# Kernel tuning notes

Hardware: AMD Instinct MI355X
Metric: run time of the kernel (lower is better)

## Reference

```python
import jax, jax.numpy as jnp
import numpy as np

B, C, H, W = 2, 128, 32, 48
D_INNER = 2 * C          # expand=2
D_STATE = 16
DT_RANK = int(np.ceil(C / 16))
K = 4                    # four scan directions
EPS = 1e-5


def setup_inputs() -> dict:
    ks = jax.random.split(jax.random.key(0), 8)
    return {
        "rgb": jax.random.normal(ks[0], (B, C, H, W), jnp.float32),
        "t": jax.random.normal(ks[1], (B, C, H, W), jnp.float32),
        "in_proj_w": jax.random.normal(ks[2], (2 * D_INNER, C), jnp.float32) / np.float32(np.sqrt(C)),
        "conv_w": jax.random.normal(ks[3], (D_INNER, 1, 3, 3), jnp.float32) / 3.0,
        "conv_b": jnp.zeros((D_INNER,), jnp.float32),
        "x_proj_w": jax.random.normal(ks[4], (K, DT_RANK + 2 * D_STATE, D_INNER), jnp.float32) / np.float32(np.sqrt(D_INNER)),
        "dt_projs_w": jax.random.normal(ks[5], (K, D_INNER, DT_RANK), jnp.float32) * np.float32(DT_RANK ** -0.5),
        "dt_projs_b": jax.random.uniform(ks[6], (K, D_INNER), jnp.float32, minval=1e-4, maxval=0.1),
        "A_logs": jnp.log(jnp.tile(jnp.arange(1, D_STATE + 1, dtype=jnp.float32), (K * D_INNER, 1))),
        "Ds": jnp.ones((K * D_INNER,), jnp.float32),
        "out_norm_g": jnp.ones((D_INNER,), jnp.float32),
        "out_norm_b": jnp.zeros((D_INNER,), jnp.float32),
        "out_proj_w": jax.random.normal(ks[7], (C, D_INNER), jnp.float32) / np.float32(np.sqrt(D_INNER)),
    }


def _selective_scan(u, delta, A, Bmat, Cmat, Dvec):
    """u, delta: (B,K,D,L); A: (K,D,N); Bmat/Cmat: (B,K,N,L); Dvec: (K,D)."""
    uT = jnp.moveaxis(u, -1, 0)      # (L,B,K,D)
    dT = jnp.moveaxis(delta, -1, 0)  # (L,B,K,D)
    BT = jnp.moveaxis(Bmat, -1, 0)   # (L,B,K,N)
    CT = jnp.moveaxis(Cmat, -1, 0)   # (L,B,K,N)
    h0 = jnp.zeros(u.shape[:3] + (A.shape[-1],), u.dtype)  # (B,K,D,N)

    def step(h, xs):
        u_t, d_t, B_t, C_t = xs
        dA = jnp.exp(d_t[..., None] * A)                       # (B,K,D,N)
        h = dA * h + (d_t * u_t)[..., None] * B_t[:, :, None, :]
        y = jnp.einsum('bkdn,bkn->bkd', h, C_t)
        return h, y

    _, ys = jax.lax.scan(step, h0, (uT, dT, BT, CT))           # ys: (L,B,K,D)
    return jnp.moveaxis(ys, 0, -1) + Dvec[None, :, :, None] * u


def _ss2d(x, in_proj_w, conv_w, conv_b, x_proj_w, dt_projs_w, dt_projs_b,
          A_logs, Ds, out_norm_g, out_norm_b, out_proj_w):
    b, hs, ws, c = x.shape
    L = hs * ws
    xz = x @ in_proj_w.T                                       # (B,Hs,Ws,2*Din)
    xx, z = jnp.split(xz, 2, axis=-1)
    xc = jnp.transpose(xx, (0, 3, 1, 2))                       # (B,Din,Hs,Ws)
    xc = jax.lax.conv_general_dilated(
        xc, conv_w, (1, 1), ((1, 1), (1, 1)),
        feature_group_count=D_INNER,
        dimension_numbers=('NCHW', 'OIHW', 'NCHW'))
    xc = jax.nn.silu(xc + conv_b[None, :, None, None])
    # 4-direction scan inputs: HW, WH, and their reverses
    x_hw = xc.reshape(b, D_INNER, L)
    x_wh = jnp.transpose(xc, (0, 1, 3, 2)).reshape(b, D_INNER, L)
    x_hwwh = jnp.stack([x_hw, x_wh], axis=1)                   # (B,2,Din,L)
    xs = jnp.concatenate([x_hwwh, jnp.flip(x_hwwh, axis=-1)], axis=1)  # (B,4,Din,L)
    x_dbl = jnp.einsum('bkdl,kcd->bkcl', xs, x_proj_w)
    dts = x_dbl[:, :, :DT_RANK]
    Bs = x_dbl[:, :, DT_RANK:DT_RANK + D_STATE]                # (B,K,N,L)
    Cs = x_dbl[:, :, DT_RANK + D_STATE:]                       # (B,K,N,L)
    dts = jnp.einsum('bkrl,kdr->bkdl', dts, dt_projs_w)
    delta = jax.nn.softplus(dts + dt_projs_b[None, :, :, None])
    A = -jnp.exp(A_logs).reshape(K, D_INNER, D_STATE)
    out_y = _selective_scan(xs, delta, A, Bs, Cs, Ds.reshape(K, D_INNER))  # (B,4,Din,L)
    inv_y = jnp.flip(out_y[:, 2:4], axis=-1)                   # (B,2,Din,L)
    wh_y = jnp.transpose(out_y[:, 1].reshape(b, D_INNER, ws, hs), (0, 1, 3, 2)).reshape(b, D_INNER, L)
    invwh_y = jnp.transpose(inv_y[:, 1].reshape(b, D_INNER, ws, hs), (0, 1, 3, 2)).reshape(b, D_INNER, L)
    y = out_y[:, 0] + inv_y[:, 0] + wh_y + invwh_y             # (B,Din,L)
    y = jnp.transpose(y, (0, 2, 1)).reshape(b, hs, ws, D_INNER)
    mu = y.mean(-1, keepdims=True)
    var = jnp.mean((y - mu) ** 2, axis=-1, keepdims=True)
    y = (y - mu) * jax.lax.rsqrt(var + EPS) * out_norm_g + out_norm_b
    y = y * jax.nn.silu(z)
    return y @ out_proj_w.T                                    # (B,Hs,Ws,C)


def reference(rgb, t, in_proj_w, conv_w, conv_b, x_proj_w, dt_projs_w, dt_projs_b,
              A_logs, Ds, out_norm_g, out_norm_b, out_proj_w):
    b, c, h, w = rgb.shape
    rgb_tok = jnp.transpose(rgb, (0, 2, 3, 1)).reshape(b, h * w, c)
    t_tok = jnp.transpose(t, (0, 2, 3, 1)).reshape(b, h * w, c)
    # interleave: rgb0, t0, rgb1, t1, ... -> (B, H, 2W, C)
    rgbt = jnp.stack([rgb_tok, t_tok], axis=2).reshape(b, h, 2 * w, c)
    out = _ss2d(rgbt, in_proj_w, conv_w, conv_b, x_proj_w, dt_projs_w, dt_projs_b,
                A_logs, Ds, out_norm_g, out_norm_b, out_proj_w)
    # keep thermal-position tokens (odd indices)
    out = out.reshape(b, 2 * h * w, c)[:, 1::2, :].reshape(b, h, w, c)
    return jnp.transpose(out, (0, 3, 1, 2))
```

## Files before the change

kernel.cpp:

```cpp
#include <hip/hip_runtime.h>

#define B_   2
#define CIN  128
#define H_   32
#define W_   48
#define HS   32
#define WS2  96
#define LT   3072
#define DI   256
#define NS   16
#define RK   8
#define KK   4
#define NCH  256
#define CHL  12

__device__ __forceinline__ int lcanon(int k, int ls) {
  if (k == 0) return ls;
  if (k == 1) return (ls & 31) * WS2 + (ls >> 5);
  if (k == 2) return LT - 1 - ls;
  int j = LT - 1 - ls;
  return (j & 31) * WS2 + (j >> 5);
}

__global__ __launch_bounds__(256) void k_wprep(
    const float* __restrict__ w, float* __restrict__ wT) {
  __shared__ float tile[32][33];
  int t = threadIdx.x;
  int bm = blockIdx.x & 15;
  int bk = blockIdx.x >> 4;
  int m0 = bm * 32, k0 = bk * 32;
  #pragma unroll
  for (int q = 0; q < 4; ++q) {
    int idx = q * 256 + t;
    int mi = idx >> 5, ki = idx & 31;
    tile[mi][ki] = w[(size_t)(m0 + mi) * CIN + k0 + ki];
  }
  __syncthreads();
  #pragma unroll
  for (int q = 0; q < 4; ++q) {
    int idx = q * 256 + t;
    int ki = idx >> 5, mi = idx & 31;
    wT[(size_t)(k0 + ki) * 512 + m0 + mi] = tile[mi][ki];
  }
}

__global__ __launch_bounds__(256) void k_inproj(
    const float* __restrict__ rgb, const float* __restrict__ tin,
    const float* __restrict__ wT, float* __restrict__ xz) {
  __shared__ float xv[CIN][16];
  int t  = threadIdx.x;
  int bi = blockIdx.x;
  bool zh = bi >= 384;
  int bb, l0;
  if (!zh) { int r = bi;       bb = r / 192; l0 = (r % 192) * 16; }
  else     { int r = bi - 384; bb = r / 96;  l0 = (r % 96) * 32; }
  int h = l0 / WS2, w20 = l0 % WS2;
  #pragma unroll
  for (int rep = 0; rep < 8; ++rep) {
    int idx = rep * 256 + t;
    int tok = idx & 15, c = idx >> 4;
    int w2 = zh ? (w20 + 2 * tok + 1) : (w20 + tok);
    const float* src = (w2 & 1) ? tin : rgb;
    xv[c][tok] = src[((size_t)(bb * CIN + c) * HS + h) * W_ + (w2 >> 1)];
  }
  __syncthreads();
  int oc = (t & 63) * 4;
  int th = t >> 6;
  const float4* wp = reinterpret_cast<const float4*>(wT + (zh ? 256 : 0) + oc);
  float4 A0 = {0,0,0,0}, A1 = {0,0,0,0}, A2 = {0,0,0,0}, A3 = {0,0,0,0};
  #pragma unroll 4
  for (int k = 0; k < CIN; ++k) {
    float4 w4 = wp[k * 128];
    float4 x4 = *reinterpret_cast<const float4*>(&xv[k][th * 4]);
    A0.x += x4.x * w4.x; A0.y += x4.x * w4.y; A0.z += x4.x * w4.z; A0.w += x4.x * w4.w;
    A1.x += x4.y * w4.x; A1.y += x4.y * w4.y; A1.z += x4.y * w4.z; A1.w += x4.y * w4.w;
    A2.x += x4.z * w4.x; A2.y += x4.z * w4.y; A2.z += x4.z * w4.z; A2.w += x4.z * w4.w;
    A3.x += x4.w * w4.x; A3.y += x4.w * w4.y; A3.z += x4.w * w4.z; A3.w += x4.w * w4.w;
  }
  int colbase = (zh ? 256 : 0) + oc;
  #pragma unroll
  for (int j = 0; j < 4; ++j) {
    int tok = th * 4 + j;
    int l = zh ? (l0 + 2 * tok + 1) : (l0 + tok);
    float4 v = (j == 0) ? A0 : (j == 1) ? A1 : (j == 2) ? A2 : A3;
    *reinterpret_cast<float4*>(xz + ((size_t)bb * LT + l) * 512 + colbase) = v;
  }
}

__global__ __launch_bounds__(256) void k_conv(
    const float* __restrict__ xz, const float* __restrict__ cw,
    const float* __restrict__ cbias, float* __restrict__ xc,
    float* __restrict__ xcT) {
  int t  = threadIdx.x;
  int bi = blockIdx.x;
  int bb = bi >> 8;
  int h  = (bi >> 3) & 31;
  int q  = bi & 7;
  int w0 = q * 12;
  float wreg[9];
  #pragma unroll
  for (int i = 0; i < 9; ++i) wreg[i] = cw[t * 9 + i];
  float bias = cbias[t];
  bool hm = (h > 0), hp = (h < HS - 1);
  const size_t rowb = ((size_t)bb * LT + h * WS2) * 512 + t;
  const size_t up = (size_t)WS2 * 512;
  float a0=0,a1=0,b0=0,b1=0,c0=0,c1=0;
  if (w0 > 0) {
    size_t o = rowb + (size_t)(w0 - 1) * 512;
    b0 = xz[o];
    if (hm) a0 = xz[o - up];
    if (hp) c0 = xz[o + up];
  }
  {
    size_t o = rowb + (size_t)w0 * 512;
    b1 = xz[o];
    if (hm) a1 = xz[o - up];
    if (hp) c1 = xz[o + up];
  }
  #pragma unroll 4
  for (int s = 0; s < 12; ++s) {
    int w2 = w0 + s;
    float a2 = 0, b2 = 0, c2 = 0;
    if (w2 + 1 < WS2) {
      size_t o = rowb + (size_t)(w2 + 1) * 512;
      b2 = xz[o];
      if (hm) a2 = xz[o - up];
      if (hp) c2 = xz[o + up];
    }
    float acc = bias
      + wreg[0]*a0 + wreg[1]*a1 + wreg[2]*a2
      + wreg[3]*b0 + wreg[4]*b1 + wreg[5]*b2
      + wreg[6]*c0 + wreg[7]*c1 + wreg[8]*c2;
    float sv = acc / (1.f + __expf(-acc));
    xc [((size_t)bb * LT + h * WS2 + w2) * DI + t] = sv;
    xcT[((size_t)bb * LT + w2 * 32 + h) * DI + t] = sv;
    a0=a1; a1=a2; b0=b1; b1=b2; c0=c1; c1=c2;
  }
}

__global__ __launch_bounds__(256) void k_deltabc(
    const float* __restrict__ xc, const float* __restrict__ xpw,
    float* __restrict__ dts_sc, float* __restrict__ Bsb, float* __restrict__ Csb) {
  __shared__ float xv[8][260];
  __shared__ float outs2[128][9];
  __shared__ float dts_s[KK][8][9];
  int t  = threadIdx.x;
  int bb = blockIdx.x / 384;
  int lt = blockIdx.x % 384;
  int l0 = lt * 8;
  #pragma unroll
  for (int i = 0; i < 8; ++i)
    xv[i][t] = xc[((size_t)bb * LT + l0 + i) * DI + t];
  __syncthreads();
  int i = t & 7, cb = t >> 3;
  float acc[5] = {0.f, 0.f, 0.f, 0.f, 0.f};
  const float4* xr  = reinterpret_cast<const float4*>(&xv[i][0]);
  const float4* wp0 = reinterpret_cast<const float4*>(xpw + (size_t)cb * DI);
  #pragma unroll 8
  for (int d4 = 0; d4 < 64; ++d4) {
    float4 x4 = xr[d4];
    #pragma unroll
    for (int j = 0; j < 5; ++j) {
      float4 w = wp0[j * 2048 + d4];
      acc[j] += w.x*x4.x + w.y*x4.y + w.z*x4.z + w.w*x4.w;
    }
  }
  #pragma unroll
  for (int j = 0; j < 5; ++j) {
    int cc  = cb + 32 * j;
    int k   = (cc * 205) >> 13;
    int c40 = cc - 40 * k;
    if (c40 < RK) dts_s[k][i][c40] = acc[j];
    else          outs2[k * 32 + (c40 - RK)][i] = acc[j];
  }
  __syncthreads();
  {
    int n = t & 15, tok = (t >> 4) & 7;
    bool isC = (t >= 128);
    int lc = l0 + tok, hh = lc / WS2, w2 = lc % WS2;
    int lw = w2 * 32 + hh;
    int lsA[4] = {lc, lw, LT - 1 - lc, LT - 1 - lw};
    float* dst = isC ? Csb : Bsb;
    int off = isC ? 16 : 0;
    #pragma unroll
    for (int k = 0; k < KK; ++k)
      dst[(((size_t)bb * KK + k) * LT + lsA[k]) * NS + n] = outs2[k * 32 + off + n][tok];
  }
  {
    int k2 = t >> 6, tok2 = (t >> 3) & 7, r = t & 7;
    int lc2 = l0 + tok2, hh2 = lc2 / WS2, w22 = lc2 % WS2;
    int lw2 = w22 * 32 + hh2;
    int ls2 = (k2 == 0) ? lc2 : (k2 == 1) ? lw2 : (k2 == 2) ? (LT - 1 - lc2) : (LT - 1 - lw2);
    dts_sc[(((size_t)bb * KK + k2) * LT + ls2) * RK + r] = dts_s[k2][tok2][r];
  }
}

#define SCAN_FRONT(S) \
    int ls = ch * CHL + (S); \
    const float4* dp = reinterpret_cast<const float4*>(dts_p + (size_t)ls * RK); \
    float4 q0 = dp[0], q1 = dp[1]; \
    float xx = bias + w0.x*q0.x + w0.y*q0.y + w0.z*q0.z + w0.w*q0.w \
                    + w1.x*q1.x + w1.y*q1.y + w1.z*q1.z + w1.w*q1.w; \
    float dlt = fmaxf(xx, 0.f) + __logf(1.f + __expf(-fabsf(xx))); \
    float du = dlt * u; \
    const float4* Bp = reinterpret_cast<const float4*>(Bsb_p + (size_t)ls * NS); \
    float4 b0 = Bp[0], b1 = Bp[1], b2 = Bp[2], b3 = Bp[3]; \
    float bv[16] = {b0.x,b0.y,b0.z,b0.w, b1.x,b1.y,b1.z,b1.w, \
                    b2.x,b2.y,b2.z,b2.w, b3.x,b3.y,b3.z,b3.w};

__global__ __launch_bounds__(256) void k_scan1(
    const float* __restrict__ dts_sc, const float* __restrict__ xc,
    const float* __restrict__ xcT, const float* __restrict__ Bsb,
    const float* __restrict__ dtw, const float* __restrict__ dtb,
    const float* __restrict__ Alog, float* __restrict__ chH,
    float* __restrict__ sumd) {
  int t  = threadIdx.x;
  int bi = blockIdx.x;
  int bb = bi / (KK * NCH);
  int k  = (bi / NCH) % KK;
  int ch = bi % NCH;
  size_t bk = (size_t)bb * KK + k;
  const float* dts_p = dts_sc + bk * LT * RK;
  const float* Bsb_p = Bsb + bk * LT * NS;
  const float* src = ((k & 1) ? xcT : xc) + (size_t)bb * LT * DI;
  int dir = (k < 2) ? 1 : -1;
  int i0  = (k < 2) ? ch * CHL : LT - 1 - ch * CHL;
  const float* wr = dtw + ((size_t)k * DI + t) * RK;
  float4 w0 = *reinterpret_cast<const float4*>(wr);
  float4 w1 = *reinterpret_cast<const float4*>(wr + 4);
  float bias = dtb[k * DI + t];
  float a[NS], h[NS];
  bool okf = true;
  #pragma unroll
  for (int n = 0; n < NS; ++n) {
    a[n] = -__expf(Alog[((size_t)k * DI + t) * NS + n]);
    h[n] = 0.f;
    if (n) okf = okf && (fabsf(a[n] - (n + 1) * a[0]) <= 1e-3f * (n + 1) * fabsf(a[0]));
  }
  float sd = 0.f;
  float u_nxt = src[(size_t)i0 * DI + t];
  if (okf) {
    for (int s = 0; s < CHL; ++s) {
      float u = u_nxt;
      int ni = (s + 1 < CHL) ? (i0 + dir * (s + 1)) : i0;
      u_nxt = src[(size_t)ni * DI + t];
      SCAN_FRONT(s)
      sd += dlt;
      float e1 = __expf(dlt * a[0]);
      float p = e1;
      #pragma unroll
      for (int n = 0; n < NS; ++n) { h[n] = p * h[n] + du * bv[n]; p *= e1; }
    }
  } else {
    for (int s = 0; s < CHL; ++s) {
      float u = u_nxt;
      int ni = (s + 1 < CHL) ? (i0 + dir * (s + 1)) : i0;
      u_nxt = src[(size_t)ni * DI + t];
      SCAN_FRONT(s)
      sd += dlt;
      #pragma unroll
      for (int n = 0; n < NS; ++n) h[n] = __expf(dlt * a[n]) * h[n] + du * bv[n];
    }
  }
  float* outp = chH + ((bk * NCH + ch) * DI + t) * NS;
  #pragma unroll
  for (int n = 0; n < NS; ++n) outp[n] = h[n];
  sumd[(bk * NCH + ch) * DI + t] = sd;
}

__global__ __launch_bounds__(256) void k_scan2(
    float* __restrict__ chH, const float* __restrict__ sumd,
    const float* __restrict__ Alog) {
  int t  = threadIdx.x;
  int bi = blockIdx.x;
  int bb = bi / (KK * 16);
  int k  = (bi / 16) % KK;
  int dg = bi % 16;
  int d = dg * 16 + (t >> 4);
  int n = t & 15;
  float a = -__expf(Alog[((size_t)k * DI + d) * NS + n]);
  float carry = 0.f;
  size_t bk = (size_t)bb * KK + k;
  size_t base = (bk * NCH) * DI + d;
  float Hc = chH[base * NS + n];
  float sd = sumd[base];
  for (int ch = 0; ch < NCH; ++ch) {
    size_t nbase = base + DI;
    float Hc2 = 0.f, sd2 = 0.f;
    if (ch + 1 < NCH) { Hc2 = chH[nbase * NS + n]; sd2 = sumd[nbase]; }
    chH[base * NS + n] = carry;
    carry = __expf(a * sd) * carry + Hc;
    base = nbase; Hc = Hc2; sd = sd2;
  }
}

__global__ __launch_bounds__(256) void k_scan3(
    const float* __restrict__ dts_sc, const float* __restrict__ xc,
    const float* __restrict__ xcT, const float* __restrict__ Bsb,
    const float* __restrict__ Csb, const float* __restrict__ dtw,
    const float* __restrict__ dtb, const float* __restrict__ Alog,
    const float* __restrict__ Ds, const float* __restrict__ chH,
    float* __restrict__ yhalf) {
  int t  = threadIdx.x;
  int bi = blockIdx.x;
  int bb = bi / (KK * NCH);
  int k  = (bi / NCH) % KK;
  int ch = bi % NCH;
  size_t bk = (size_t)bb * KK + k;
  const float* dts_p = dts_sc + bk * LT * RK;
  const float* Bsb_p = Bsb + bk * LT * NS;
  const float* Csb_p = Csb + bk * LT * NS;
  const float* src = ((k & 1) ? xcT : xc) + (size_t)bb * LT * DI;
  int dir = (k < 2) ? 1 : -1;
  int i0  = (k < 2) ? ch * CHL : LT - 1 - ch * CHL;
  const float* wr = dtw + ((size_t)k * DI + t) * RK;
  float4 w0 = *reinterpret_cast<const float4*>(wr);
  float4 w1 = *reinterpret_cast<const float4*>(wr + 4);
  float bias = dtb[k * DI + t];
  float a[NS], h[NS];
  bool okf = true;
  #pragma unroll
  for (int n = 0; n < NS; ++n) {
    a[n] = -__expf(Alog[((size_t)k * DI + t) * NS + n]);
    if (n) okf = okf && (fabsf(a[n] - (n + 1) * a[0]) <= 1e-3f * (n + 1) * fabsf(a[0]));
  }
  const float4* hp = reinterpret_cast<const float4*>(chH + ((bk * NCH + ch) * DI + t) * NS);
  float4 h0 = hp[0], h1 = hp[1], h2 = hp[2], h3 = hp[3];
  {
    float tmp[16] = {h0.x,h0.y,h0.z,h0.w, h1.x,h1.y,h1.z,h1.w,
                     h2.x,h2.y,h2.z,h2.w, h3.x,h3.y,h3.z,h3.w};
    #pragma unroll
    for (int n = 0; n < NS; ++n) h[n] = tmp[n];
  }
  float dv = Ds[k * DI + t];
  float u_nxt = src[(size_t)i0 * DI + t];
  if (okf) {
    for (int s = 0; s < CHL; ++s) {
      float u = u_nxt;
      int ni = (s + 1 < CHL) ? (i0 + dir * (s + 1)) : i0;
      u_nxt = src[(size_t)ni * DI + t];
      SCAN_FRONT(s)
      const float4* Cp = reinterpret_cast<const float4*>(Csb_p + (size_t)ls * NS);
      float4 c0 = Cp[0], c1 = Cp[1], c2 = Cp[2], c3 = Cp[3];
      float cv[16] = {c0.x,c0.y,c0.z,c0.w, c1.x,c1.y,c1.z,c1.w,
                      c2.x,c2.y,c2.z,c2.w, c3.x,c3.y,c3.z,c3.w};
      float e1 = __expf(dlt * a[0]);
      float p = e1;
      float y = 0.f;
      #pragma unroll
      for (int n = 0; n < NS; ++n) { h[n] = p * h[n] + du * bv[n]; y += h[n] * cv[n]; p *= e1; }
      y += dv * u;
      int lc = lcanon(k, ls);
      if (lc & 1)
        yhalf[(bk * (LT/2) + (lc >> 1)) * DI + t] = y;
    }
  } else {
    for (int s = 0; s < CHL; ++s) {
      float u = u_nxt;
      int ni = (s + 1 < CHL) ? (i0 + dir * (s + 1)) : i0;
      u_nxt = src[(size_t)ni * DI + t];
      SCAN_FRONT(s)
      const float4* Cp = reinterpret_cast<const float4*>(Csb_p + (size_t)ls * NS);
      float4 c0 = Cp[0], c1 = Cp[1], c2 = Cp[2], c3 = Cp[3];
      float cv[16] = {c0.x,c0.y,c0.z,c0.w, c1.x,c1.y,c1.z,c1.w,
                      c2.x,c2.y,c2.z,c2.w, c3.x,c3.y,c3.z,c3.w};
      float y = 0.f;
      #pragma unroll
      for (int n = 0; n < NS; ++n) { h[n] = __expf(dlt * a[n]) * h[n] + du * bv[n]; y += h[n] * cv[n]; }
      y += dv * u;
      int lc = lcanon(k, ls);
      if (lc & 1)
        yhalf[(bk * (LT/2) + (lc >> 1)) * DI + t] = y;
    }
  }
}

__global__ __launch_bounds__(256) void k_out(
    const float* __restrict__ yhalf, const float* __restrict__ xz,
    const float* __restrict__ gam, const float* __restrict__ be,
    const float* __restrict__ opw, float* __restrict__ out) {
  __shared__ float yt[4][260];
  int t = threadIdx.x;
  int bb   = blockIdx.x / 384;
  int tile = blockIdx.x % 384;
  {
    int lane = t & 63, tok = t >> 6;
    int m = tile * 4 + tok;
    int lc = (m / W_) * WS2 + (m % W_) * 2 + 1;
    float yv[4];
    #pragma unroll
    for (int j = 0; j < 4; ++j) {
      int d = lane + 64 * j;
      float s = 0.f;
      #pragma unroll
      for (int k = 0; k < KK; ++k)
        s += yhalf[(((size_t)bb * KK + k) * (LT/2) + m) * DI + d];
      yv[j] = s;
    }
    float sum = yv[0] + yv[1] + yv[2] + yv[3];
    #pragma unroll
    for (int off = 32; off > 0; off >>= 1) sum += __shfl_xor(sum, off, 64);
    float mu = sum * (1.f / DI);
    float sq = 0.f;
    #pragma unroll
    for (int j = 0; j < 4; ++j) { float dd = yv[j] - mu; sq += dd * dd; }
    #pragma unroll
    for (int off = 32; off > 0; off >>= 1) sq += __shfl_xor(sq, off, 64);
    float rs = rsqrtf(sq * (1.f / DI) + 1e-5f);
    #pragma unroll
    for (int j = 0; j < 4; ++j) {
      int d = lane + 64 * j;
      float z = xz[((size_t)bb * LT + lc) * 512 + DI + d];
      float sz = z / (1.f + __expf(-z));
      yt[tok][d] = ((yv[j] - mu) * rs * gam[d] + be[d]) * sz;
    }
  }
  __syncthreads();
  int i = t & 3, og = t >> 2;
  const float4* yr = reinterpret_cast<const float4*>(&yt[i][0]);
  const float4* w0p = reinterpret_cast<const float4*>(opw + (size_t)og * DI);
  const float4* w1p = reinterpret_cast<const float4*>(opw + (size_t)(og + 64) * DI);
  float a0 = 0.f, a1 = 0.f;
  for (int d4 = 0; d4 < 64; ++d4) {
    float4 y4 = yr[d4];
    float4 wa = w0p[d4], wb2 = w1p[d4];
    a0 += wa.x*y4.x + wa.y*y4.y + wa.z*y4.z + wa.w*y4.w;
    a1 += wb2.x*y4.x + wb2.y*y4.y + wb2.z*y4.z + wb2.w*y4.w;
  }
  int m = tile * 4 + i;
  int hh = m / W_, ww = m % W_;
  out[((size_t)(bb * CIN + og) * HS + hh) * W_ + ww] = a0;
  out[((size_t)(bb * CIN + og + 64) * HS + hh) * W_ + ww] = a1;
}

extern "C" void kernel_launch(void* const* d_in, const int* in_sizes, int n_in,
                              void* d_out, int out_size, void* d_ws, size_t ws_size,
                              hipStream_t stream) {
  const float* rgb  = (const float*)d_in[0];
  const float* tin  = (const float*)d_in[1];
  const float* ipw  = (const float*)d_in[2];
  const float* cw   = (const float*)d_in[3];
  const float* cb   = (const float*)d_in[4];
  const float* xpw  = (const float*)d_in[5];
  const float* dtw  = (const float*)d_in[6];
  const float* dtb  = (const float*)d_in[7];
  const float* Alog = (const float*)d_in[8];
  const float* Ds   = (const float*)d_in[9];
  const float* g    = (const float*)d_in[10];
  const float* be   = (const float*)d_in[11];
  const float* opw  = (const float*)d_in[12];
  float* out = (float*)d_out;

  float* ws    = (float*)d_ws;
  float* xz    = ws;
  float* xc    = xz    + 3145728;
  float* xcT   = xc    + 1572864;
  float* dts   = xcT   + 1572864;
  float* Bsb   = dts   + 393216;
  float* Csb   = Bsb   + 393216;
  float* chH   = Csb   + 393216;
  float* sumd  = chH   + 8388608;
  float* yhalf = sumd  + 524288;
  float* wT    = yhalf + 3145728;

  k_wprep  <<<64,   256, 0, stream>>>(ipw, wT);
  k_inproj <<<576,  256, 0, stream>>>(rgb, tin, wT, xz);
  k_conv   <<<512,  256, 0, stream>>>(xz, cw, cb, xc, xcT);
  k_deltabc<<<768,  256, 0, stream>>>(xc, xpw, dts, Bsb, Csb);
  k_scan1  <<<2048, 256, 0, stream>>>(dts, xc, xcT, Bsb, dtw, dtb, Alog, chH, sumd);
  k_scan2  <<<128,  256, 0, stream>>>(chH, sumd, Alog);
  k_scan3  <<<2048, 256, 0, stream>>>(dts, xc, xcT, Bsb, Csb, dtw, dtb, Alog, Ds, chH, yhalf);
  k_out    <<<768,  256, 0, stream>>>(yhalf, xz, g, be, opw, out);
}
```

Measured before the change: 161.4 us.

## Store scan chunk states and partial outputs in bf16, halve chunk count

Stores the per-chunk scan states (chH) and the per-direction partial outputs (yhalf) as bf16 instead of fp32, using round-to-nearest-even packing, which halves their memory traffic in scan1, scan2, scan3 and the output kernel. It also doubles the chunk length and halves the chunk count, so the sequential carry pass in scan2 has half the steps and less intermediate state is written. The cost is lower precision in the inter-chunk carries and the summed outputs, and fewer blocks in scan1 and scan3, each doing a longer serial loop. The workspace offsets are reshuffled to match the smaller buffers.

```diff
diff --git a/kernel.cpp b/kernel.cpp
--- a/kernel.cpp
+++ b/kernel.cpp
@@ -11,8 +11,19 @@
 #define NS   16
 #define RK   8
 #define KK   4
-#define NCH  256
-#define CHL  12
+#define NCH  128
+#define CHL  24
+
+typedef unsigned int  u32;
+typedef unsigned short u16;
+
+__device__ __forceinline__ u16 f2bf(float x) {
+  u32 u = __float_as_uint(x);
+  return (u16)((u + 0x7FFFu + ((u >> 16) & 1u)) >> 16);
+}
+__device__ __forceinline__ float bf2f(u16 s) {
+  return __uint_as_float((u32)s << 16);
+}
 
 __device__ __forceinline__ int lcanon(int k, int ls) {
   if (k == 0) return ls;
@@ -212,7 +223,7 @@
     const float* __restrict__ dts_sc, const float* __restrict__ xc,
     const float* __restrict__ xcT, const float* __restrict__ Bsb,
     const float* __restrict__ dtw, const float* __restrict__ dtb,
-    const float* __restrict__ Alog, float* __restrict__ chH,
+    const float* __restrict__ Alog, u16* __restrict__ chH,
     float* __restrict__ sumd) {
   int t  = threadIdx.x;
   int bi = blockIdx.x;
@@ -262,14 +273,18 @@
       for (int n = 0; n < NS; ++n) h[n] = __expf(dlt * a[n]) * h[n] + du * bv[n];
     }
   }
-  float* outp = chH + ((bk * NCH + ch) * DI + t) * NS;
-  #pragma unroll
-  for (int n = 0; n < NS; ++n) outp[n] = h[n];
+  u32 pk[8];
+  #pragma unroll
+  for (int i = 0; i < 8; ++i)
+    pk[i] = (u32)f2bf(h[2*i]) | ((u32)f2bf(h[2*i+1]) << 16);
+  u32* outp = reinterpret_cast<u32*>(chH + ((bk * NCH + ch) * DI + t) * NS);
+  *reinterpret_cast<uint4*>(outp)     = make_uint4(pk[0], pk[1], pk[2], pk[3]);
+  *reinterpret_cast<uint4*>(outp + 4) = make_uint4(pk[4], pk[5], pk[6], pk[7]);
   sumd[(bk * NCH + ch) * DI + t] = sd;
 }
 
 __global__ __launch_bounds__(256) void k_scan2(
-    float* __restrict__ chH, const float* __restrict__ sumd,
+    u16* __restrict__ chH, const float* __restrict__ sumd,
     const float* __restrict__ Alog) {
   int t  = threadIdx.x;
   int bi = blockIdx.x;
@@ -282,13 +297,13 @@
   float carry = 0.f;
   size_t bk = (size_t)bb * KK + k;
   size_t base = (bk * NCH) * DI + d;
-  float Hc = chH[base * NS + n];
+  float Hc = bf2f(chH[base * NS + n]);
   float sd = sumd[base];
   for (int ch = 0; ch < NCH; ++ch) {
     size_t nbase = base + DI;
     float Hc2 = 0.f, sd2 = 0.f;
-    if (ch + 1 < NCH) { Hc2 = chH[nbase * NS + n]; sd2 = sumd[nbase]; }
-    chH[base * NS + n] = carry;
+    if (ch + 1 < NCH) { Hc2 = bf2f(chH[nbase * NS + n]); sd2 = sumd[nbase]; }
+    chH[base * NS + n] = f2bf(carry);
     carry = __expf(a * sd) * carry + Hc;
     base = nbase; Hc = Hc2; sd = sd2;
   }
@@ -299,8 +314,8 @@
     const float* __restrict__ xcT, const float* __restrict__ Bsb,
     const float* __restrict__ Csb, const float* __restrict__ dtw,
     const float* __restrict__ dtb, const float* __restrict__ Alog,
-    const float* __restrict__ Ds, const float* __restrict__ chH,
-    float* __restrict__ yhalf) {
+    const float* __restrict__ Ds, const u16* __restrict__ chH,
+    u16* __restrict__ yhalf) {
   int t  = threadIdx.x;
   int bi = blockIdx.x;
   int bb = bi / (KK * NCH);
@@ -324,13 +339,15 @@
     a[n] = -__expf(Alog[((size_t)k * DI + t) * NS + n]);
     if (n) okf = okf && (fabsf(a[n] - (n + 1) * a[0]) <= 1e-3f * (n + 1) * fabsf(a[0]));
   }
-  const float4* hp = reinterpret_cast<const float4*>(chH + ((bk * NCH + ch) * DI + t) * NS);
-  float4 h0 = hp[0], h1 = hp[1], h2 = hp[2], h3 = hp[3];
   {
-    float tmp[16] = {h0.x,h0.y,h0.z,h0.w, h1.x,h1.y,h1.z,h1.w,
-                     h2.x,h2.y,h2.z,h2.w, h3.x,h3.y,h3.z,h3.w};
-    #pragma unroll
-    for (int n = 0; n < NS; ++n) h[n] = tmp[n];
+    const uint4* hp4 = reinterpret_cast<const uint4*>(chH + ((bk * NCH + ch) * DI + t) * NS);
+    uint4 A = hp4[0], Bq = hp4[1];
+    u32 w[8] = {A.x, A.y, A.z, A.w, Bq.x, Bq.y, Bq.z, Bq.w};
+    #pragma unroll
+    for (int i = 0; i < 8; ++i) {
+      h[2*i]   = bf2f((u16)(w[i] & 0xFFFFu));
+      h[2*i+1] = bf2f((u16)(w[i] >> 16));
+    }
   }
   float dv = Ds[k * DI + t];
   float u_nxt = src[(size_t)i0 * DI + t];
@@ -352,7 +369,7 @@
       y += dv * u;
       int lc = lcanon(k, ls);
       if (lc & 1)
-        yhalf[(bk * (LT/2) + (lc >> 1)) * DI + t] = y;
+        yhalf[(bk * (LT/2) + (lc >> 1)) * DI + t] = f2bf(y);
     }
   } else {
     for (int s = 0; s < CHL; ++s) {
@@ -370,13 +387,13 @@
       y += dv * u;
       int lc = lcanon(k, ls);
       if (lc & 1)
-        yhalf[(bk * (LT/2) + (lc >> 1)) * DI + t] = y;
+        yhalf[(bk * (LT/2) + (lc >> 1)) * DI + t] = f2bf(y);
     }
   }
 }
 
 __global__ __launch_bounds__(256) void k_out(
-    const float* __restrict__ yhalf, const float* __restrict__ xz,
+    const u16* __restrict__ yhalf, const float* __restrict__ xz,
     const float* __restrict__ gam, const float* __restrict__ be,
     const float* __restrict__ opw, float* __restrict__ out) {
   __shared__ float yt[4][260];
@@ -394,7 +411,7 @@
       float s = 0.f;
       #pragma unroll
       for (int k = 0; k < KK; ++k)
-        s += yhalf[(((size_t)bb * KK + k) * (LT/2) + m) * DI + d];
+        s += bf2f(yhalf[(((size_t)bb * KK + k) * (LT/2) + m) * DI + d]);
       yv[j] = s;
     }
     float sum = yv[0] + yv[1] + yv[2] + yv[3];
@@ -456,19 +473,19 @@
   float* xc    = xz    + 3145728;
   float* xcT   = xc    + 1572864;
   float* dts   = xcT   + 1572864;
-  float* Bsb   = dts   + 393216;
+  float* Bsb   = dts   + 196608;
   float* Csb   = Bsb   + 393216;
-  float* chH   = Csb   + 393216;
-  float* sumd  = chH   + 8388608;
-  float* yhalf = sumd  + 524288;
-  float* wT    = yhalf + 3145728;
+  u16*   chH   = (u16*)(Csb + 393216);
+  float* sumd  = Csb   + 393216 + 2097152;
+  u16*   yhalf = (u16*)(sumd + 262144);
+  float* wT    = sumd  + 262144 + 1572864;
 
   k_wprep  <<<64,   256, 0, stream>>>(ipw, wT);
   k_inproj <<<576,  256, 0, stream>>>(rgb, tin, wT, xz);
   k_conv   <<<512,  256, 0, stream>>>(xz, cw, cb, xc, xcT);
   k_deltabc<<<768,  256, 0, stream>>>(xc, xpw, dts, Bsb, Csb);
-  k_scan1  <<<2048, 256, 0, stream>>>(dts, xc, xcT, Bsb, dtw, dtb, Alog, chH, sumd);
+  k_scan1  <<<1024, 256, 0, stream>>>(dts, xc, xcT, Bsb, dtw, dtb, Alog, chH, sumd);
   k_scan2  <<<128,  256, 0, stream>>>(chH, sumd, Alog);
-  k_scan3  <<<2048, 256, 0, stream>>>(dts, xc, xcT, Bsb, Csb, dtw, dtb, Alog, Ds, chH, yhalf);
+  k_scan3  <<<1024, 256, 0, stream>>>(dts, xc, xcT, Bsb, Csb, dtw, dtb, Alog, Ds, chH, yhalf);
   k_out    <<<768,  256, 0, stream>>>(yhalf, xz, g, be, opw, out);
 }
```

After: 156.6 us. -3.0%, faster.
